# Optimization experiments

Hardware: AMD Instinct MI355X
Metric: run time of the kernel (lower is better)

## Reference

```python
import jax, jax.numpy as jnp
import numpy as np

N_HEAD, D_MODEL, D_K, D_V = 16, 1024, 64, 64
LN_EPS = 1e-5


def setup_inputs() -> dict:
    key = jax.random.key(0)
    ks = jax.random.split(key, 10)
    B, S = 2, 2048
    s = 1.0 / np.sqrt(D_MODEL)
    return {
        "q": jax.random.normal(ks[0], (B, S, D_MODEL), jnp.float32),
        "k": jax.random.normal(ks[1], (B, S, D_MODEL), jnp.float32),
        "v": jax.random.normal(ks[2], (B, S, D_MODEL), jnp.float32),
        "w_q": jax.random.normal(ks[3], (D_MODEL, N_HEAD * D_K), jnp.float32) * s,
        "w_k": jax.random.normal(ks[4], (D_MODEL, N_HEAD * D_K), jnp.float32) * s,
        "w_v": jax.random.normal(ks[5], (D_MODEL, N_HEAD * D_V), jnp.float32) * s,
        "w_fc": jax.random.normal(ks[6], (N_HEAD * D_V, D_MODEL), jnp.float32) * s,
        "b_fc": jnp.zeros((D_MODEL,), jnp.float32),
        "ln_g": jnp.ones((D_MODEL,), jnp.float32),
        "ln_b": jnp.zeros((D_MODEL,), jnp.float32),
    }


def _mha(q, k, v, w_q, w_k, w_v, w_fc, b_fc, ln_g, ln_b):
    B, S, _ = q.shape
    residual = q
    # projections -> [B, H, S, Dh]
    qh = (q @ w_q).reshape(B, S, N_HEAD, D_K).transpose(0, 2, 1, 3)
    kh = (k @ w_k).reshape(B, S, N_HEAD, D_K).transpose(0, 2, 1, 3)
    vh = (v @ w_v).reshape(B, S, N_HEAD, D_V).transpose(0, 2, 1, 3)
    # NOTE: original scales by sqrt(d_model), not sqrt(d_k)
    temper = jnp.sqrt(jnp.asarray(D_MODEL, qh.dtype))
    attn = jnp.einsum("bhqd,bhkd->bhqk", qh, kh) / temper
    attn = jax.nn.softmax(attn, axis=-1)  # dropout = identity (eval mode)
    out = jnp.einsum("bhqk,bhkd->bhqd", attn, vh)
    out = out.transpose(0, 2, 1, 3).reshape(B, S, N_HEAD * D_V)
    out = out @ w_fc + b_fc  # dropout = identity (eval mode)
    x = out + residual
    mu = jnp.mean(x, axis=-1, keepdims=True)
    var = jnp.var(x, axis=-1, keepdims=True)
    x = (x - mu) * jax.lax.rsqrt(var + LN_EPS) * ln_g + ln_b
    return x, attn


def reference(q, k, v, w_q, w_k, w_v, w_fc, b_fc, ln_g, ln_b):
    return _mha(q, k, v, w_q, w_k, w_v, w_fc, b_fc, ln_g, ln_b)
```

## Files before the change

kernel.cpp:

```cpp
#include <hip/hip_runtime.h>
#include <hip/hip_bf16.h>
#include <stdint.h>

typedef __attribute__((ext_vector_type(8))) short bf16x8;
typedef __attribute__((ext_vector_type(4))) float f32x4;

#define GLOAD16(gptr, lptr)                                              \
  __builtin_amdgcn_global_load_lds(                                      \
      (const __attribute__((address_space(1))) void*)(gptr),             \
      (__attribute__((address_space(3))) void*)(lptr), 16, 0, 0)

__device__ __forceinline__ uint32_t pack_bf16_2(float a, float b) {
  union { __hip_bfloat16 h; unsigned short u; } ca, cb;
  ca.h = __float2bfloat16(a); cb.h = __float2bfloat16(b);
  return (uint32_t)ca.u | ((uint32_t)cb.u << 16);
}

__global__ __launch_bounds__(256)
void cvt_kernel(const float* __restrict__ in0, const float* __restrict__ in1,
                const float* __restrict__ in2, __hip_bfloat16* __restrict__ out0,
                __hip_bfloat16* __restrict__ out1, __hip_bfloat16* __restrict__ out2,
                int n)
{
  const int z = blockIdx.y;
  const float* in = z == 0 ? in0 : z == 1 ? in1 : in2;
  __hip_bfloat16* out = z == 0 ? out0 : z == 1 ? out1 : out2;
  long i = ((long)blockIdx.x * 256 + threadIdx.x) * 8;
  if (i + 8 > n) return;
  float4 a = *(const float4*)(in + i);
  float4 b = *(const float4*)(in + i + 4);
  uint4 r;
  r.x = pack_bf16_2(a.x, a.y); r.y = pack_bf16_2(a.z, a.w);
  r.z = pack_bf16_2(b.x, b.y); r.w = pack_bf16_2(b.z, b.w);
  *(uint4*)(out + i) = r;
}

__global__ __launch_bounds__(256)
void wtrans_kernel(const float* __restrict__ w0, const float* __restrict__ w1,
                   const float* __restrict__ w2, const float* __restrict__ w3,
                   __hip_bfloat16* __restrict__ o0, __hip_bfloat16* __restrict__ o1,
                   __hip_bfloat16* __restrict__ o2, __hip_bfloat16* __restrict__ o3)
{
  const int z = blockIdx.z;
  const float* in = z == 0 ? w0 : z == 1 ? w1 : z == 2 ? w2 : w3;
  __hip_bfloat16* out = z == 0 ? o0 : z == 1 ? o1 : z == 2 ? o2 : o3;
  __shared__ float t[64][65];
  const int tx = threadIdx.x & 15, ty = threadIdx.x >> 4;
  const int bx = blockIdx.x, by = blockIdx.y;
  for (int i = 0; i < 4; ++i)
    for (int j = 0; j < 4; ++j)
      t[ty*4+i][tx*4+j] = in[(long)(by*64 + ty*4+i)*1024 + bx*64 + tx*4 + j];
  __syncthreads();
  for (int i = 0; i < 4; ++i)
    for (int j = 0; j < 4; ++j)
      out[(long)(bx*64 + ty*4+i)*1024 + by*64 + tx*4 + j] =
          __float2bfloat16(t[tx*4+j][ty*4+i]);
}

__global__ __launch_bounds__(256)
void vtrans_kernel(const __hip_bfloat16* __restrict__ in, __hip_bfloat16* __restrict__ out)
{
  __shared__ __hip_bfloat16 t[64][72];
  const int tx = threadIdx.x & 15, ty = threadIdx.x >> 4;
  const int sb = blockIdx.x, bh = blockIdx.y;
  const __hip_bfloat16* inp = in + (long)bh * 2048 * 64;
  __hip_bfloat16* outp = out + (long)bh * 64 * 2048;
  for (int i = 0; i < 4; ++i)
    for (int j = 0; j < 4; ++j)
      t[ty*4+i][tx*4+j] = inp[(long)(sb*64 + ty*4+i)*64 + tx*4 + j];
  __syncthreads();
  for (int i = 0; i < 4; ++i)
    for (int j = 0; j < 4; ++j)
      outp[(long)(ty*4+i)*2048 + sb*64 + tx*4 + j] = t[tx*4+j][ty*4+i];
}

template<int EPI>
__global__ __launch_bounds__(256)
void gemm_bt(const __hip_bfloat16* __restrict__ A0,
             const __hip_bfloat16* __restrict__ A1,
             const __hip_bfloat16* __restrict__ A2,
             const __hip_bfloat16* __restrict__ B0,
             const __hip_bfloat16* __restrict__ B1,
             const __hip_bfloat16* __restrict__ B2,
             void* __restrict__ out,
             const float* __restrict__ bias,
             const float* __restrict__ resid,
             int M, int N, int K)
{
  const int z = (EPI == 0) ? blockIdx.z : 0;
  const __hip_bfloat16* A  = z == 0 ? A0 : z == 1 ? A1 : A2;
  const __hip_bfloat16* Bt = z == 0 ? B0 : z == 1 ? B1 : B2;
  const float scale = (EPI == 0 && z == 0) ? 0.045084219f : 1.0f;

  __shared__ __hip_bfloat16 As[128*32];
  __shared__ __hip_bfloat16 Bs[128*32];
  const int tid = threadIdx.x;
  const int wid = tid >> 6;
  const int lane = tid & 63;
  const int lr = lane & 15, lg = lane >> 4;
  const int bm = blockIdx.y, bn = blockIdx.x;
  const int wm = wid >> 1, wn = wid & 1;

  f32x4 acc[4][4] = {};

  const int srow = tid >> 2;
  const int scol = (tid & 3) * 8;
  const __hip_bfloat16* Ag = A  + (long)(bm*128 + srow)*K + scol;
  const __hip_bfloat16* Bg = Bt + (long)(bn*128 + srow)*K + scol;
  __hip_bfloat16* AsW = &As[wid*512];
  __hip_bfloat16* BsW = &Bs[wid*512];

  for (int k0 = 0; k0 < K; k0 += 32) {
    GLOAD16(Ag + k0,          AsW);
    GLOAD16(Ag + 64*K + k0,   AsW + 2048);
    GLOAD16(Bg + k0,          BsW);
    GLOAD16(Bg + 64*K + k0,   BsW + 2048);
    __syncthreads();
    bf16x8 a[4], b[4];
    for (int m = 0; m < 4; ++m)
      a[m] = *(const bf16x8*)&As[(wm*64 + m*16 + lr)*32 + lg*8];
    for (int n = 0; n < 4; ++n)
      b[n] = *(const bf16x8*)&Bs[(wn*64 + n*16 + lr)*32 + lg*8];
    for (int m = 0; m < 4; ++m)
      for (int n = 0; n < 4; ++n)
        acc[m][n] = __builtin_amdgcn_mfma_f32_16x16x32_bf16(b[n], a[m], acc[m][n], 0, 0, 0);
    __syncthreads();
  }

  for (int m = 0; m < 4; ++m) {
    const int grow = bm*128 + wm*64 + m*16 + lr;
    for (int n = 0; n < 4; ++n) {
      const int c0 = bn*128 + wn*64 + n*16 + lg*4;
      if (EPI == 0) {
        const int b_ = grow >> 11, s = grow & 2047;
        const int h = c0 >> 6, d = c0 & 63;
        uint2 pk;
        pk.x = pack_bf16_2(acc[m][n][0]*scale, acc[m][n][1]*scale);
        pk.y = pack_bf16_2(acc[m][n][2]*scale, acc[m][n][3]*scale);
        *(uint2*)((__hip_bfloat16*)out + (long)z*4194304 +
                  ((long)(b_*16 + h)*2048 + s)*64 + d) = pk;
      } else {
        float4 b4 = *(const float4*)(bias + c0);
        float4 r4 = *(const float4*)(resid + (long)grow*N + c0);
        float4 o4;
        o4.x = acc[m][n][0] + b4.x + r4.x;
        o4.y = acc[m][n][1] + b4.y + r4.y;
        o4.z = acc[m][n][2] + b4.z + r4.z;
        o4.w = acc[m][n][3] + b4.w + r4.w;
        *(float4*)((float*)out + (long)grow*N + c0) = o4;
      }
    }
  }
}

__global__ __launch_bounds__(256)
void attn_kernel(const __hip_bfloat16* __restrict__ Qh,
                 const __hip_bfloat16* __restrict__ Kh,
                 const __hip_bfloat16* __restrict__ Vt,
                 float* __restrict__ attn_out,
                 __hip_bfloat16* __restrict__ O)
{
  __shared__ __hip_bfloat16 Ps[64*128];
  __shared__ float red[4][64];
  __shared__ float invl[64];

  const int tid = threadIdx.x, wid = tid >> 6, lane = tid & 63;
  const int lr = lane & 15, lg = lane >> 4;
  const int qb = blockIdx.x, bh = blockIdx.y;

  const __hip_bfloat16* Qlane = Qh + ((long)bh*2048 + qb*64 + lr)*64 + lg*8;
  const __hip_bfloat16* Klane = Kh + (long)bh*2048*64 + (long)(wid*32 + lr)*64 + lg*8;
  const __hip_bfloat16* Vlane = Vt + (long)bh*64*2048 + (long)(wid*16 + lr)*2048 + lg*8;

  bf16x8 aq[4][2];
  for (int mq = 0; mq < 4; ++mq)
    for (int kk = 0; kk < 2; ++kk)
      aq[mq][kk] = *(const bf16x8*)(Qlane + mq*1024 + kk*32);

  float rs[4] = {0.f, 0.f, 0.f, 0.f};
  for (int kt = 0; kt < 16; ++kt) {
    bf16x8 bk[2][2];
    for (int nk = 0; nk < 2; ++nk)
      for (int kk = 0; kk < 2; ++kk)
        bk[nk][kk] = *(const bf16x8*)(Klane + kt*8192 + nk*1024 + kk*32);
    f32x4 s2[4][2] = {};
    for (int mq = 0; mq < 4; ++mq)
      for (int nk = 0; nk < 2; ++nk)
        for (int kk = 0; kk < 2; ++kk)
          s2[mq][nk] = __builtin_amdgcn_mfma_f32_16x16x32_bf16(bk[nk][kk], aq[mq][kk], s2[mq][nk], 0, 0, 0);
    for (int mq = 0; mq < 4; ++mq)
      for (int nk = 0; nk < 2; ++nk)
        for (int jj = 0; jj < 4; ++jj)
          rs[mq] += exp2f(s2[mq][nk][jj]);
  }

  for (int mq = 0; mq < 4; ++mq) {
    float e = rs[mq];
    e += __shfl_xor(e, 16);
    e += __shfl_xor(e, 32);
    rs[mq] = e;
  }
  if (lg == 0)
    for (int mq = 0; mq < 4; ++mq)
      red[wid][mq*16 + lr] = rs[mq];
  __syncthreads();
  if (tid < 64)
    invl[tid] = 1.0f / (red[0][tid] + red[1][tid] + red[2][tid] + red[3][tid]);
  __syncthreads();

  float iv[4];
  for (int mq = 0; mq < 4; ++mq) iv[mq] = invl[mq*16 + lr];

  f32x4 acc_o[4] = {};
  float* attn_row = attn_out + ((long)bh*2048 + qb*64)*2048;

  for (int kt = 0; kt < 16; ++kt) {
    bf16x8 bk[2][2];
    for (int nk = 0; nk < 2; ++nk)
      for (int kk = 0; kk < 2; ++kk)
        bk[nk][kk] = *(const bf16x8*)(Klane + kt*8192 + nk*1024 + kk*32);
    bf16x8 vb[4];
    for (int k2 = 0; k2 < 4; ++k2)
      vb[k2] = *(const bf16x8*)(Vlane + kt*128 + k2*32);

    f32x4 s2[4][2] = {};
    for (int mq = 0; mq < 4; ++mq)
      for (int nk = 0; nk < 2; ++nk)
        for (int kk = 0; kk < 2; ++kk)
          s2[mq][nk] = __builtin_amdgcn_mfma_f32_16x16x32_bf16(bk[nk][kk], aq[mq][kk], s2[mq][nk], 0, 0, 0);

    for (int mq = 0; mq < 4; ++mq) {
      const int row = mq*16 + lr;
      for (int nk = 0; nk < 2; ++nk) {
        const int kc = wid*32 + nk*16 + lg*4;
        f32x4 p;
        p[0] = exp2f(s2[mq][nk][0]) * iv[mq];
        p[1] = exp2f(s2[mq][nk][1]) * iv[mq];
        p[2] = exp2f(s2[mq][nk][2]) * iv[mq];
        p[3] = exp2f(s2[mq][nk][3]) * iv[mq];
        __builtin_nontemporal_store(p, (f32x4*)(attn_row + (long)row*2048 + kt*128 + kc));
        uint2 pb;
        pb.x = pack_bf16_2(p[0], p[1]);
        pb.y = pack_bf16_2(p[2], p[3]);
        const int boff = (row*256 + kc*2) ^ ((row & 15) << 4);
        *(uint2*)((char*)Ps + boff) = pb;
      }
    }
    __syncthreads();

    for (int mq = 0; mq < 4; ++mq) {
      const int row = mq*16 + lr;
      for (int k2 = 0; k2 < 4; ++k2) {
        const int boff = (row*256 + (k2*32 + lg*8)*2) ^ ((row & 15) << 4);
        bf16x8 pa = *(const bf16x8*)((char*)Ps + boff);
        acc_o[mq] = __builtin_amdgcn_mfma_f32_16x16x32_bf16(vb[k2], pa, acc_o[mq], 0, 0, 0);
      }
    }
    __syncthreads();
  }

  const int b_ = bh >> 4, h = bh & 15;
  for (int mq = 0; mq < 4; ++mq) {
    const long grow = (long)b_*2048 + qb*64 + mq*16 + lr;
    const int col = h*64 + wid*16 + lg*4;
    uint2 pk;
    pk.x = pack_bf16_2(acc_o[mq][0], acc_o[mq][1]);
    pk.y = pack_bf16_2(acc_o[mq][2], acc_o[mq][3]);
    *(uint2*)(O + grow*1024 + col) = pk;
  }
}

__global__ __launch_bounds__(256)
void ln_kernel(const float* __restrict__ xin, const float* __restrict__ gam,
               const float* __restrict__ bet, float* __restrict__ xout)
{
  const int row = blockIdx.x;
  const int tid = threadIdx.x;
  const float* xr = xin + (long)row*1024;
  float4 v = *(const float4*)(xr + tid*4);
  float s  = v.x + v.y + v.z + v.w;
  float ss = v.x*v.x + v.y*v.y + v.z*v.z + v.w*v.w;
  for (int o = 1; o < 64; o <<= 1) {
    s  += __shfl_xor(s, o, 64);
    ss += __shfl_xor(ss, o, 64);
  }
  __shared__ float rsh[4], rssh[4];
  const int wid = tid >> 6, lane = tid & 63;
  if (lane == 0) { rsh[wid] = s; rssh[wid] = ss; }
  __syncthreads();
  s  = rsh[0] + rsh[1] + rsh[2] + rsh[3];
  ss = rssh[0] + rssh[1] + rssh[2] + rssh[3];
  const float mean = s * (1.0f/1024.0f);
  const float var  = ss * (1.0f/1024.0f) - mean*mean;
  const float rstd = rsqrtf(var + 1e-5f);
  float4 g4 = *(const float4*)(gam + tid*4);
  float4 b4 = *(const float4*)(bet + tid*4);
  float4 o4;
  o4.x = (v.x - mean)*rstd*g4.x + b4.x;
  o4.y = (v.y - mean)*rstd*g4.y + b4.y;
  o4.z = (v.z - mean)*rstd*g4.z + b4.z;
  o4.w = (v.w - mean)*rstd*g4.w + b4.w;
  *(float4*)(xout + (long)row*1024 + tid*4) = o4;
}

extern "C" void kernel_launch(void* const* d_in, const int* in_sizes, int n_in,
                              void* d_out, int out_size, void* d_ws, size_t ws_size,
                              hipStream_t stream)
{
  (void)in_sizes; (void)n_in; (void)out_size; (void)ws_size;
  const float* q    = (const float*)d_in[0];
  const float* k    = (const float*)d_in[1];
  const float* v    = (const float*)d_in[2];
  const float* w_q  = (const float*)d_in[3];
  const float* w_k  = (const float*)d_in[4];
  const float* w_v  = (const float*)d_in[5];
  const float* w_fc = (const float*)d_in[6];
  const float* b_fc = (const float*)d_in[7];
  const float* ln_g = (const float*)d_in[8];
  const float* ln_b = (const float*)d_in[9];

  const long MB = 1024*1024;
  char* ws = (char*)d_ws;
  __hip_bfloat16* q_bf  = (__hip_bfloat16*)(ws);
  __hip_bfloat16* k_bf  = (__hip_bfloat16*)(ws +  8*MB);
  __hip_bfloat16* v_bf  = (__hip_bfloat16*)(ws + 16*MB);
  __hip_bfloat16* wq_t  = (__hip_bfloat16*)(ws + 24*MB);
  __hip_bfloat16* wk_t  = (__hip_bfloat16*)(ws + 26*MB);
  __hip_bfloat16* wv_t  = (__hip_bfloat16*)(ws + 28*MB);
  __hip_bfloat16* wfc_t = (__hip_bfloat16*)(ws + 30*MB);
  __hip_bfloat16* QKVh  = (__hip_bfloat16*)(ws + 32*MB);
  __hip_bfloat16* Qh    = QKVh;
  __hip_bfloat16* Kh    = QKVh + 4194304L;
  __hip_bfloat16* Vh    = QKVh + 8388608L;
  __hip_bfloat16* Vht   = (__hip_bfloat16*)(ws + 56*MB);
  __hip_bfloat16* Obuf  = (__hip_bfloat16*)(ws + 64*MB);
  float*          xbuf  = (float*)(ws + 72*MB);

  float* x_out    = (float*)d_out;
  float* attn_out = x_out + 4194304L;

  const int NQ = 4096*1024;
  cvt_kernel<<<dim3(NQ/2048, 3), 256, 0, stream>>>(q, k, v, q_bf, k_bf, v_bf, NQ);

  wtrans_kernel<<<dim3(16, 16, 4), 256, 0, stream>>>(w_q, w_k, w_v, w_fc,
                                                     wq_t, wk_t, wv_t, wfc_t);

  gemm_bt<0><<<dim3(8, 32, 3), 256, 0, stream>>>(q_bf, k_bf, v_bf,
                                                 wq_t, wk_t, wv_t,
                                                 QKVh, nullptr, nullptr, 4096, 1024, 1024);

  vtrans_kernel<<<dim3(32, 32), 256, 0, stream>>>(Vh, Vht);

  attn_kernel<<<dim3(32, 32), 256, 0, stream>>>(Qh, Kh, Vht, attn_out, Obuf);

  gemm_bt<2><<<dim3(8, 32), 256, 0, stream>>>(Obuf, nullptr, nullptr,
                                              wfc_t, nullptr, nullptr,
                                              xbuf, b_fc, q, 4096, 1024, 1024);

  ln_kernel<<<4096, 256, 0, stream>>>(xbuf, ln_g, ln_b, x_out);
}
```

Before: 288.6 us.

## Merge prep kernels, remap attention blocks, add priority hints and occupancy bound

Combines the activation bf16 conversion and the weight transpose into one launch, which removes one kernel boundary. The attention grid is flattened and remapped so consecutive block IDs are spread across (bh, qb) in a strided pattern, presumably to spread work across XCDs and L2. The attention kernel also gets a minimum-occupancy launch bound, s_setprio around its MFMA sections, and explicit unroll pragmas (with unroll 1 on the kt loop). The occupancy bound may force register spills, and the remap could hurt K/V locality.

```diff
diff --git a/kernel.cpp b/kernel.cpp
--- a/kernel.cpp
+++ b/kernel.cpp
@@ -17,44 +17,45 @@
 }
 
 __global__ __launch_bounds__(256)
-void cvt_kernel(const float* __restrict__ in0, const float* __restrict__ in1,
-                const float* __restrict__ in2, __hip_bfloat16* __restrict__ out0,
-                __hip_bfloat16* __restrict__ out1, __hip_bfloat16* __restrict__ out2,
-                int n)
-{
-  const int z = blockIdx.y;
-  const float* in = z == 0 ? in0 : z == 1 ? in1 : in2;
-  __hip_bfloat16* out = z == 0 ? out0 : z == 1 ? out1 : out2;
-  long i = ((long)blockIdx.x * 256 + threadIdx.x) * 8;
-  if (i + 8 > n) return;
-  float4 a = *(const float4*)(in + i);
-  float4 b = *(const float4*)(in + i + 4);
-  uint4 r;
-  r.x = pack_bf16_2(a.x, a.y); r.y = pack_bf16_2(a.z, a.w);
-  r.z = pack_bf16_2(b.x, b.y); r.w = pack_bf16_2(b.z, b.w);
-  *(uint4*)(out + i) = r;
-}
-
-__global__ __launch_bounds__(256)
-void wtrans_kernel(const float* __restrict__ w0, const float* __restrict__ w1,
-                   const float* __restrict__ w2, const float* __restrict__ w3,
-                   __hip_bfloat16* __restrict__ o0, __hip_bfloat16* __restrict__ o1,
-                   __hip_bfloat16* __restrict__ o2, __hip_bfloat16* __restrict__ o3)
-{
-  const int z = blockIdx.z;
-  const float* in = z == 0 ? w0 : z == 1 ? w1 : z == 2 ? w2 : w3;
-  __hip_bfloat16* out = z == 0 ? o0 : z == 1 ? o1 : z == 2 ? o2 : o3;
-  __shared__ float t[64][65];
-  const int tx = threadIdx.x & 15, ty = threadIdx.x >> 4;
-  const int bx = blockIdx.x, by = blockIdx.y;
-  for (int i = 0; i < 4; ++i)
-    for (int j = 0; j < 4; ++j)
-      t[ty*4+i][tx*4+j] = in[(long)(by*64 + ty*4+i)*1024 + bx*64 + tx*4 + j];
-  __syncthreads();
-  for (int i = 0; i < 4; ++i)
-    for (int j = 0; j < 4; ++j)
-      out[(long)(bx*64 + ty*4+i)*1024 + by*64 + tx*4 + j] =
-          __float2bfloat16(t[tx*4+j][ty*4+i]);
+void prep_kernel(const float* __restrict__ q, const float* __restrict__ k,
+                 const float* __restrict__ v,
+                 __hip_bfloat16* __restrict__ q_bf, __hip_bfloat16* __restrict__ k_bf,
+                 __hip_bfloat16* __restrict__ v_bf,
+                 const float* __restrict__ w0, const float* __restrict__ w1,
+                 const float* __restrict__ w2, const float* __restrict__ w3,
+                 __hip_bfloat16* __restrict__ o0, __hip_bfloat16* __restrict__ o1,
+                 __hip_bfloat16* __restrict__ o2, __hip_bfloat16* __restrict__ o3)
+{
+  const int blk = blockIdx.x;
+  if (blk < 6144) {
+    const int z = blk >> 11;
+    const int bx = blk & 2047;
+    const float* in = z == 0 ? q : z == 1 ? k : v;
+    __hip_bfloat16* out = z == 0 ? q_bf : z == 1 ? k_bf : v_bf;
+    long i = ((long)bx * 256 + threadIdx.x) * 8;
+    float4 a = *(const float4*)(in + i);
+    float4 b = *(const float4*)(in + i + 4);
+    uint4 r;
+    r.x = pack_bf16_2(a.x, a.y); r.y = pack_bf16_2(a.z, a.w);
+    r.z = pack_bf16_2(b.x, b.y); r.w = pack_bf16_2(b.z, b.w);
+    *(uint4*)(out + i) = r;
+  } else {
+    __shared__ float t[64][65];
+    const int w = blk - 6144;
+    const int z = w >> 8;
+    const int by = (w >> 4) & 15, bx = w & 15;
+    const float* in = z == 0 ? w0 : z == 1 ? w1 : z == 2 ? w2 : w3;
+    __hip_bfloat16* out = z == 0 ? o0 : z == 1 ? o1 : z == 2 ? o2 : o3;
+    const int tx = threadIdx.x & 15, ty = threadIdx.x >> 4;
+    for (int i = 0; i < 4; ++i)
+      for (int j = 0; j < 4; ++j)
+        t[ty*4+i][tx*4+j] = in[(long)(by*64 + ty*4+i)*1024 + bx*64 + tx*4 + j];
+    __syncthreads();
+    for (int i = 0; i < 4; ++i)
+      for (int j = 0; j < 4; ++j)
+        out[(long)(bx*64 + ty*4+i)*1024 + by*64 + tx*4 + j] =
+            __float2bfloat16(t[tx*4+j][ty*4+i]);
+  }
 }
 
 __global__ __launch_bounds__(256)
@@ -153,7 +154,7 @@
   }
 }
 
-__global__ __launch_bounds__(256)
+__global__ __launch_bounds__(256, 4)
 void attn_kernel(const __hip_bfloat16* __restrict__ Qh,
                  const __hip_bfloat16* __restrict__ Kh,
                  const __hip_bfloat16* __restrict__ Vt,
@@ -166,7 +167,8 @@
 
   const int tid = threadIdx.x, wid = tid >> 6, lane = tid & 63;
   const int lr = lane & 15, lg = lane >> 4;
-  const int qb = blockIdx.x, bh = blockIdx.y;
+  const int orig = (blockIdx.x & 7) * 128 + (blockIdx.x >> 3);
+  const int bh = orig >> 5, qb = orig & 31;
 
   const __hip_bfloat16* Qlane = Qh + ((long)bh*2048 + qb*64 + lr)*64 + lg*8;
   const __hip_bfloat16* Klane = Kh + (long)bh*2048*64 + (long)(wid*32 + lr)*64 + lg*8;
@@ -214,21 +216,27 @@
   f32x4 acc_o[4] = {};
   float* attn_row = attn_out + ((long)bh*2048 + qb*64)*2048;
 
+#pragma unroll 1
   for (int kt = 0; kt < 16; ++kt) {
-    bf16x8 bk[2][2];
+    bf16x8 bk[2][2], vb[4];
+#pragma unroll
     for (int nk = 0; nk < 2; ++nk)
       for (int kk = 0; kk < 2; ++kk)
         bk[nk][kk] = *(const bf16x8*)(Klane + kt*8192 + nk*1024 + kk*32);
-    bf16x8 vb[4];
+#pragma unroll
     for (int k2 = 0; k2 < 4; ++k2)
       vb[k2] = *(const bf16x8*)(Vlane + kt*128 + k2*32);
 
     f32x4 s2[4][2] = {};
+    __builtin_amdgcn_s_setprio(1);
+#pragma unroll
     for (int mq = 0; mq < 4; ++mq)
       for (int nk = 0; nk < 2; ++nk)
         for (int kk = 0; kk < 2; ++kk)
           s2[mq][nk] = __builtin_amdgcn_mfma_f32_16x16x32_bf16(bk[nk][kk], aq[mq][kk], s2[mq][nk], 0, 0, 0);
-
+    __builtin_amdgcn_s_setprio(0);
+
+#pragma unroll
     for (int mq = 0; mq < 4; ++mq) {
       const int row = mq*16 + lr;
       for (int nk = 0; nk < 2; ++nk) {
@@ -248,6 +256,8 @@
     }
     __syncthreads();
 
+    __builtin_amdgcn_s_setprio(1);
+#pragma unroll
     for (int mq = 0; mq < 4; ++mq) {
       const int row = mq*16 + lr;
       for (int k2 = 0; k2 < 4; ++k2) {
@@ -256,6 +266,7 @@
         acc_o[mq] = __builtin_amdgcn_mfma_f32_16x16x32_bf16(vb[k2], pa, acc_o[mq], 0, 0, 0);
       }
     }
+    __builtin_amdgcn_s_setprio(0);
     __syncthreads();
   }
 
@@ -339,11 +350,9 @@
   float* x_out    = (float*)d_out;
   float* attn_out = x_out + 4194304L;
 
-  const int NQ = 4096*1024;
-  cvt_kernel<<<dim3(NQ/2048, 3), 256, 0, stream>>>(q, k, v, q_bf, k_bf, v_bf, NQ);
-
-  wtrans_kernel<<<dim3(16, 16, 4), 256, 0, stream>>>(w_q, w_k, w_v, w_fc,
-                                                     wq_t, wk_t, wv_t, wfc_t);
+  prep_kernel<<<7168, 256, 0, stream>>>(q, k, v, q_bf, k_bf, v_bf,
+                                        w_q, w_k, w_v, w_fc,
+                                        wq_t, wk_t, wv_t, wfc_t);
 
   gemm_bt<0><<<dim3(8, 32, 3), 256, 0, stream>>>(q_bf, k_bf, v_bf,
                                                  wq_t, wk_t, wv_t,
@@ -351,7 +360,7 @@
 
   vtrans_kernel<<<dim3(32, 32), 256, 0, stream>>>(Vh, Vht);
 
-  attn_kernel<<<dim3(32, 32), 256, 0, stream>>>(Qh, Kh, Vht, attn_out, Obuf);
+  attn_kernel<<<1024, 256, 0, stream>>>(Qh, Kh, Vht, attn_out, Obuf);
 
   gemm_bt<2><<<dim3(8, 32), 256, 0, stream>>>(Obuf, nullptr, nullptr,
                                               wfc_t, nullptr, nullptr,
```

Result: slower. 310.6 us (+7.6%).
